# Kernel tuning notes

Measured on AMD Instinct MI355X. Metric: run time of the kernel, lower is better.

## Reference

```python
import jax, jax.numpy as jnp
import numpy as np

T, B, IN = 512, 256, 64
INNER = 20


def _lin_params(key, fan_in, fan_out):
    k1, k2 = jax.random.split(key)
    bound = 1.0 / np.sqrt(fan_in)
    w = jax.random.uniform(k1, (fan_out, fan_in), jnp.float32, -bound, bound)
    b = jax.random.uniform(k2, (fan_out,), jnp.float32, -bound, bound)
    return w, b


def _rnn_params(key, in_sz, hid):
    k1, k2, k3, k4 = jax.random.split(key, 4)
    bound = 1.0 / np.sqrt(hid)
    wih = jax.random.uniform(k1, (hid, in_sz), jnp.float32, -bound, bound)
    whh = jax.random.uniform(k2, (hid, hid), jnp.float32, -bound, bound)
    bih = jax.random.uniform(k3, (hid,), jnp.float32, -bound, bound)
    bhh = jax.random.uniform(k4, (hid,), jnp.float32, -bound, bound)
    return wih, whh, bih, bhh


def setup_inputs() -> dict:
    key = jax.random.key(0)
    ks = jax.random.split(key, 9)
    x = jax.random.normal(ks[0], (T, B, IN), jnp.float32)
    e_w1, e_b1 = _lin_params(ks[1], IN, 128)
    e_w2, e_b2 = _lin_params(ks[2], 128, 64)
    e_w3, e_b3 = _lin_params(ks[3], 64, 32)
    r1_wih, r1_whh, r1_bih, r1_bhh = _rnn_params(ks[4], 32, INNER)
    r2_wih, r2_whh, r2_bih, r2_bhh = _rnn_params(ks[5], INNER, 32)
    d_w1, d_b1 = _lin_params(ks[6], 32, 64)
    d_w2, d_b2 = _lin_params(ks[7], 64, 128)
    d_w3, d_b3 = _lin_params(ks[8], 128, IN)
    return dict(x=x,
                e_w1=e_w1, e_b1=e_b1, e_w2=e_w2, e_b2=e_b2, e_w3=e_w3, e_b3=e_b3,
                r1_wih=r1_wih, r1_whh=r1_whh, r1_bih=r1_bih, r1_bhh=r1_bhh,
                r2_wih=r2_wih, r2_whh=r2_whh, r2_bih=r2_bih, r2_bhh=r2_bhh,
                d_w1=d_w1, d_b1=d_b1, d_w2=d_w2, d_b2=d_b2, d_w3=d_w3, d_b3=d_b3)


def _rnn(x, wih, whh, bih, bhh):
    # x: (T, B, F); vanilla tanh RNN, h0 = 0. Returns all hidden states (T, B, H).
    # Precompute input projection for all timesteps in one GEMM.
    xp = jnp.einsum('tbf,hf->tbh', x, wih) + bih + bhh
    h0 = jnp.zeros((x.shape[1], whh.shape[0]), x.dtype)

    def step(h, xt):
        h = jnp.tanh(xt + h @ whh.T)
        return h, h

    _, out = jax.lax.scan(step, h0, xp)
    return out


def reference(x,
              e_w1, e_b1, e_w2, e_b2, e_w3, e_b3,
              r1_wih, r1_whh, r1_bih, r1_bhh,
              r2_wih, r2_whh, r2_bih, r2_bhh,
              d_w1, d_b1, d_w2, d_b2, d_w3, d_b3):
    relu = jax.nn.relu
    # encoder MLP
    h = relu(x @ e_w1.T + e_b1)
    h = relu(h @ e_w2.T + e_b2)
    h = relu(h @ e_w3.T + e_b3)
    # encoder RNN -> code (T, B, INNER)
    code = _rnn(h, r1_wih, r1_whh, r1_bih, r1_bhh)
    # decoder RNN then ReLU
    d = relu(_rnn(code, r2_wih, r2_whh, r2_bih, r2_bhh))
    d = relu(d @ d_w1.T + d_b1)
    d = relu(d @ d_w2.T + d_b2)
    return d @ d_w3.T + d_b3
```

## Files before the change

### kernel.cpp

```cpp
#include <hip/hip_runtime.h>

typedef _Float16 half8 __attribute__((ext_vector_type(8)));
typedef _Float16 half2_t __attribute__((ext_vector_type(2)));
typedef float f32x4 __attribute__((ext_vector_type(4)));

#define MFMA16(a, b, c) __builtin_amdgcn_mfma_f32_16x16x32_f16((a), (b), (c), 0, 0, 0)

__device__ __forceinline__ float exp2_fast(float x) {
#if __has_builtin(__builtin_amdgcn_exp2f)
    return __builtin_amdgcn_exp2f(x);
#else
    return exp2f(x);
#endif
}

__device__ __forceinline__ float tanh_fast(float x) {
    x = fminf(x, 22.f);
    float e = exp2_fast(2.885390082f * x);
    return (e - 1.f) * __builtin_amdgcn_rcpf(e + 1.f);
}

__device__ __forceinline__ float dot2f(unsigned a, unsigned b, float c) {
#if __has_builtin(__builtin_amdgcn_fdot2)
    return __builtin_amdgcn_fdot2(__builtin_bit_cast(half2_t, a),
                                  __builtin_bit_cast(half2_t, b), c, false);
#else
    float d;
    asm("v_dot2_f32_f16 %0, %1, %2, %3" : "=v"(d) : "v"(a), "v"(b), "v"(c));
    return d;
#endif
}


__global__ __launch_bounds__(256) void prep_kernel(
    const float* __restrict__ e_w1, const float* __restrict__ e_w3,
    const float* __restrict__ r1_wih, const float* __restrict__ e_w2,
    const float* __restrict__ d_w1, const float* __restrict__ d_w2,
    const float* __restrict__ d_w3,
    const float* __restrict__ r1_whh, const float* __restrict__ r2_wih,
    const float* __restrict__ r2_whh,
    const float* __restrict__ r2_bih, const float* __restrict__ r2_bhh,
    _Float16* __restrict__ enc_img, _Float16* __restrict__ w2img,
    _Float16* __restrict__ dec_img, _Float16* __restrict__ dw3img,
    unsigned* __restrict__ rnn_img)
{
    int i = blockIdx.x * 256 + threadIdx.x;
    if (i < 8192) {
        int r = i >> 6, c = i & 63;
        enc_img[r * 72 + c] = (_Float16)e_w1[i];
    } else if (i < 10240) {
        int j = i - 8192; int r = j >> 6, c = j & 63;
        enc_img[9216 + r * 72 + c] = (_Float16)e_w3[j];
    } else if (i < 10880) {
        int j = i - 10240; int r = j >> 5, c = j & 31;
        enc_img[11520 + r * 40 + c] = (_Float16)r1_wih[j];
    } else if (i < 19072) {
        int j = i - 10880;
        w2img[j] = (_Float16)e_w2[j];
    } else if (i < 21120) {
        int j = i - 19072; int r = j >> 5, c = j & 31;
        dec_img[r * 40 + c] = (_Float16)d_w1[j];
    } else if (i < 29312) {
        int j = i - 21120; int r = j >> 6, c = j & 63;
        dec_img[2560 + r * 72 + c] = (_Float16)d_w2[j];
    } else if (i < 37504) {
        int j = i - 29312;
        dw3img[j] = (_Float16)d_w3[j];
    } else if (i < 39552) {
        int j = i - 37504;
        int row = j >> 5, c = j & 31;
        unsigned val = 0;
        if (c == 26) {
            float b = (row < 32) ? (r2_bih[row] + r2_bhh[row]) : 0.f;
            val = __builtin_bit_cast(unsigned, b);
        } else {
            float v0 = 0.f, v1 = 0.f;
            if (row < 32) {
                if (c < 10)      { v0 = r2_wih[row * 20 + 2*c]; v1 = r2_wih[row * 20 + 2*c + 1]; }
                else if (c < 26) { int k = c - 10;
                                   v0 = r2_whh[row * 32 + 2*k]; v1 = r2_whh[row * 32 + 2*k + 1]; }
            } else if (row < 52) {
                int uu = row - 32;
                if (c < 10)      { v0 = r1_whh[uu * 20 + 2*c]; v1 = r1_whh[uu * 20 + 2*c + 1]; }
            }
            unsigned lo = (unsigned)__builtin_bit_cast(unsigned short, (_Float16)v0);
            unsigned hi = (unsigned)__builtin_bit_cast(unsigned short, (_Float16)v1);
            val = lo | (hi << 16);
        }
        rnn_img[j] = val;
    }
}

__global__ __launch_bounds__(256) void enc_kernel(
    const float* __restrict__ x,
    const float* __restrict__ eb1, const float* __restrict__ eb2,
    const float* __restrict__ eb3,
    const float* __restrict__ r1bih, const float* __restrict__ r1bhh,
    const _Float16* __restrict__ enc_img, const _Float16* __restrict__ w2img,
    float* __restrict__ xp1)
{
    extern __shared__ char smem[];
    _Float16* Wl    = (_Float16*)smem;
    _Float16* a2buf = (_Float16*)(smem + 25600);
    _Float16* a1buf = (_Float16*)(smem + 34816);
    _Float16* a3buf = (_Float16*)(smem + 52224);

    const int tid = threadIdx.x;
    {
        const uint4* src = (const uint4*)enc_img;
        uint4* dst = (uint4*)smem;
        #pragma unroll
        for (int i = 0; i < 7; ++i) {
            int idx = i * 256 + tid;
            if (idx < 1600) dst[idx] = src[idx];
        }
    }
    __syncthreads();

    const int lane = tid & 63;
    const int wv   = tid >> 6;
    const int l15  = lane & 15;
    const int kg   = lane >> 4;
    const int rowA  = blockIdx.x * 64 + wv * 16 + l15;
    const int rowDl = wv * 16 + kg * 4;
    const int rowDg = blockIdx.x * 64 + rowDl;

    half8 a0, a1f;
    {
        const float* xr = x + (size_t)rowA * 64 + kg * 8;
        f32x4 p0 = *(const f32x4*)(xr);
        f32x4 p1 = *(const f32x4*)(xr + 4);
        f32x4 p2 = *(const f32x4*)(xr + 32);
        f32x4 p3 = *(const f32x4*)(xr + 36);
        #pragma unroll
        for (int j = 0; j < 4; ++j) {
            a0[j]    = (_Float16)p0[j];
            a0[j+4]  = (_Float16)p1[j];
            a1f[j]   = (_Float16)p2[j];
            a1f[j+4] = (_Float16)p3[j];
        }
    }
    f32x4 acc1[8] = {};
    #pragma unroll
    for (int ct = 0; ct < 8; ++ct) {
        const _Float16* wp = Wl + (ct * 16 + l15) * 72 + kg * 8;
        half8 b0 = *(const half8*)(wp);
        half8 b1 = *(const half8*)(wp + 32);
        acc1[ct] = MFMA16(a0, b0, acc1[ct]);
        acc1[ct] = MFMA16(a1f, b1, acc1[ct]);
    }
    #pragma unroll
    for (int ct = 0; ct < 8; ++ct) {
        int col = ct * 16 + l15;
        float b = eb1[col];
        #pragma unroll
        for (int r = 0; r < 4; ++r) {
            float v = fmaxf(acc1[ct][r] + b, 0.f);
            a1buf[(rowDl + r) * 136 + col] = (_Float16)v;
        }
    }
    __syncthreads();

    half8 af[4];
    #pragma unroll
    for (int kt = 0; kt < 4; ++kt)
        af[kt] = *(const half8*)(a1buf + (wv * 16 + l15) * 136 + kt * 32 + kg * 8);
    f32x4 acc2[4] = {};
    #pragma unroll
    for (int ct = 0; ct < 4; ++ct) {
        const _Float16* wp = w2img + (ct * 16 + l15) * 128 + kg * 8;
        #pragma unroll
        for (int kt = 0; kt < 4; ++kt) {
            half8 b = *(const half8*)(wp + kt * 32);
            acc2[ct] = MFMA16(af[kt], b, acc2[ct]);
        }
    }
    #pragma unroll
    for (int ct = 0; ct < 4; ++ct) {
        int col = ct * 16 + l15;
        float b = eb2[col];
        #pragma unroll
        for (int r = 0; r < 4; ++r) {
            float v = fmaxf(acc2[ct][r] + b, 0.f);
            a2buf[(rowDl + r) * 72 + col] = (_Float16)v;
        }
    }
    __syncthreads();

    half8 c0 = *(const half8*)(a2buf + (wv * 16 + l15) * 72 + kg * 8);
    half8 c1 = *(const half8*)(a2buf + (wv * 16 + l15) * 72 + 32 + kg * 8);
    f32x4 acc3[2] = {};
    #pragma unroll
    for (int ct = 0; ct < 2; ++ct) {
        const _Float16* wp = Wl + 9216 + (ct * 16 + l15) * 72 + kg * 8;
        half8 b0 = *(const half8*)(wp);
        half8 b1 = *(const half8*)(wp + 32);
        acc3[ct] = MFMA16(c0, b0, acc3[ct]);
        acc3[ct] = MFMA16(c1, b1, acc3[ct]);
    }
    #pragma unroll
    for (int ct = 0; ct < 2; ++ct) {
        int col = ct * 16 + l15;
        float b = eb3[col];
        #pragma unroll
        for (int r = 0; r < 4; ++r) {
            float v = fmaxf(acc3[ct][r] + b, 0.f);
            a3buf[(rowDl + r) * 40 + col] = (_Float16)v;
        }
    }
    __syncthreads();

    half8 d0 = *(const half8*)(a3buf + (wv * 16 + l15) * 40 + kg * 8);
    f32x4 acc4[2] = {};
    #pragma unroll
    for (int ct = 0; ct < 2; ++ct) {
        const _Float16* wp = Wl + 11520 + (ct * 16 + l15) * 40 + kg * 8;
        half8 b0 = *(const half8*)(wp);
        acc4[ct] = MFMA16(d0, b0, acc4[ct]);
    }
    #pragma unroll
    for (int ct = 0; ct < 2; ++ct) {
        int col = ct * 16 + l15;
        if (col < 20) {
            float bs = r1bih[col] + r1bhh[col];
            #pragma unroll
            for (int r = 0; r < 4; ++r)
                xp1[(size_t)(rowDg + r) * 20 + col] = acc4[ct][r] + bs;
        }
    }
}

__global__ __launch_bounds__(64) void rnn_kernel(
    const float* __restrict__ xp1,
    const unsigned* __restrict__ rnn_img,
    _Float16* __restrict__ dbuf)
{
    const int lane  = threadIdx.x & 63;
    const int batch = blockIdx.x;

    unsigned w[26];
    float base_b;
    {
        const unsigned* wr = rnn_img + lane * 32;
        #pragma unroll
        for (int i = 0; i < 6; ++i) {
            uint4 q = *(const uint4*)(wr + i * 4);
            w[i*4+0] = q.x; w[i*4+1] = q.y; w[i*4+2] = q.z; w[i*4+3] = q.w;
        }
        uint4 q = *(const uint4*)(wr + 24);
        w[24] = q.x; w[25] = q.y;
        base_b = __builtin_bit_cast(float, q.z);
    }

    const bool isB = lane < 32;
    int ua = lane - 32;
    if (ua < 0 || ua > 19) ua = 0;
    const float* xcol = xp1 + (size_t)batch * 20 + ua;

    const size_t DUMP_ELEMS = 4198400;
    _Float16* dst = isB ? (dbuf + (size_t)batch * 32 + lane)
                        : (dbuf + DUMP_ELEMS + (size_t)batch * 64 + lane);
    const size_t dstride = isB ? 8192 : 0;

    const unsigned sel = (lane & 1) ? 0x01000504u : 0x05040100u;
    unsigned hs[26];

    {
        float x0 = xcol[0];
        float h0 = isB ? 0.f : tanh_fast(x0);
        _Float16 h16 = (_Float16)h0;
        unsigned own  = (unsigned)__builtin_bit_cast(unsigned short, h16);
        unsigned dppv = (unsigned)__builtin_amdgcn_update_dpp(0, (int)own, 0xB1, 0xF, 0xF, false);
        unsigned pk   = __builtin_amdgcn_perm(dppv, own, sel);
        #pragma unroll
        for (int i = 0; i < 10; ++i) hs[i]    = (unsigned)__builtin_amdgcn_readlane((int)pk, 32 + 2*i);
        #pragma unroll
        for (int i = 0; i < 16; ++i) hs[10+i] = (unsigned)__builtin_amdgcn_readlane((int)pk, 2*i);
    }

    float xr[8];
    #pragma unroll
    for (int j = 0; j < 8; ++j)
        xr[j] = xcol[(size_t)(1 + j) * 5120];

    #pragma unroll 1
    for (int t0 = 0; t0 < 512; t0 += 8) {
        #pragma unroll
        for (int j = 0; j < 8; ++j) {
            const int t = t0 + j;
            float a0 = isB ? base_b : xr[j];
            float a1 = 0.f, a2 = 0.f, a3 = 0.f, a4 = 0.f, a5 = 0.f, a6 = 0.f, a7 = 0.f;
            a0 = dot2f(w[0],  hs[0],  a0);
            a1 = dot2f(w[1],  hs[1],  a1);
            a2 = dot2f(w[2],  hs[2],  a2);
            a3 = dot2f(w[3],  hs[3],  a3);
            a4 = dot2f(w[4],  hs[4],  a4);
            a5 = dot2f(w[5],  hs[5],  a5);
            a6 = dot2f(w[6],  hs[6],  a6);
            a7 = dot2f(w[7],  hs[7],  a7);
            a0 = dot2f(w[8],  hs[8],  a0);
            a1 = dot2f(w[9],  hs[9],  a1);
            a2 = dot2f(w[10], hs[10], a2);
            a3 = dot2f(w[11], hs[11], a3);
            a4 = dot2f(w[12], hs[12], a4);
            a5 = dot2f(w[13], hs[13], a5);
            a6 = dot2f(w[14], hs[14], a6);
            a7 = dot2f(w[15], hs[15], a7);
            a0 = dot2f(w[16], hs[16], a0);
            a1 = dot2f(w[17], hs[17], a1);
            a2 = dot2f(w[18], hs[18], a2);
            a3 = dot2f(w[19], hs[19], a3);
            a4 = dot2f(w[20], hs[20], a4);
            a5 = dot2f(w[21], hs[21], a5);
            a6 = dot2f(w[22], hs[22], a6);
            a7 = dot2f(w[23], hs[23], a7);
            a0 = dot2f(w[24], hs[24], a0);
            a1 = dot2f(w[25], hs[25], a1);
            float r = ((a0 + a1) + (a2 + a3)) + ((a4 + a5) + (a6 + a7));
            float h = tanh_fast(r);
            _Float16 h16 = (_Float16)h;

            _Float16 z = (_Float16)0.f;
            *dst = (h16 > z) ? h16 : z;
            dst += dstride;

            unsigned own  = (unsigned)__builtin_bit_cast(unsigned short, h16);
            unsigned dppv = (unsigned)__builtin_amdgcn_update_dpp(0, (int)own, 0xB1, 0xF, 0xF, false);
            unsigned pk   = __builtin_amdgcn_perm(dppv, own, sel);
            #pragma unroll
            for (int i = 0; i < 10; ++i) hs[i]    = (unsigned)__builtin_amdgcn_readlane((int)pk, 32 + 2*i);
            #pragma unroll
            for (int i = 0; i < 16; ++i) hs[10+i] = (unsigned)__builtin_amdgcn_readlane((int)pk, 2*i);

            xr[j] = xcol[(size_t)(t + 9) * 5120];
        }
    }
}

__global__ __launch_bounds__(256) void dec_kernel(
    const _Float16* __restrict__ dbuf,
    const float* __restrict__ db1, const float* __restrict__ db2,
    const float* __restrict__ db3,
    const _Float16* __restrict__ dec_img, const _Float16* __restrict__ dw3img,
    float* __restrict__ out)
{
    extern __shared__ char smem[];
    _Float16* Wl    = (_Float16*)smem;
    _Float16* a1buf = (_Float16*)(smem + 23552);
    _Float16* a2buf = (_Float16*)(smem + 32768);

    const int tid = threadIdx.x;
    {
        const uint4* src = (const uint4*)dec_img;
        uint4* dst = (uint4*)smem;
        #pragma unroll
        for (int i = 0; i < 6; ++i) {
            int idx = i * 256 + tid;
            if (idx < 1472) dst[idx] = src[idx];
        }
    }
    __syncthreads();

    const int lane = tid & 63;
    const int wv   = tid >> 6;
    const int l15  = lane & 15;
    const int kg   = lane >> 4;
    const int rowA  = blockIdx.x * 64 + wv * 16 + l15;
    const int rowDl = wv * 16 + kg * 4;
    const int rowDg = blockIdx.x * 64 + rowDl;

    half8 a0 = *(const half8*)(dbuf + (size_t)rowA * 32 + kg * 8);
    f32x4 acc1[4] = {};
    #pragma unroll
    for (int ct = 0; ct < 4; ++ct) {
        half8 b = *(const half8*)(Wl + (ct * 16 + l15) * 40 + kg * 8);
        acc1[ct] = MFMA16(a0, b, acc1[ct]);
    }
    #pragma unroll
    for (int ct = 0; ct < 4; ++ct) {
        int col = ct * 16 + l15;
        float b = db1[col];
        #pragma unroll
        for (int r = 0; r < 4; ++r) {
            float v = fmaxf(acc1[ct][r] + b, 0.f);
            a1buf[(rowDl + r) * 72 + col] = (_Float16)v;
        }
    }
    __syncthreads();

    half8 af0 = *(const half8*)(a1buf + (wv * 16 + l15) * 72 + kg * 8);
    half8 af1 = *(const half8*)(a1buf + (wv * 16 + l15) * 72 + 32 + kg * 8);
    f32x4 acc2[8] = {};
    #pragma unroll
    for (int ct = 0; ct < 8; ++ct) {
        const _Float16* wp = Wl + 2560 + (ct * 16 + l15) * 72 + kg * 8;
        half8 b0 = *(const half8*)(wp);
        half8 b1 = *(const half8*)(wp + 32);
        acc2[ct] = MFMA16(af0, b0, acc2[ct]);
        acc2[ct] = MFMA16(af1, b1, acc2[ct]);
    }
    #pragma unroll
    for (int ct = 0; ct < 8; ++ct) {
        int col = ct * 16 + l15;
        float b = db2[col];
        #pragma unroll
        for (int r = 0; r < 4; ++r) {
            float v = fmaxf(acc2[ct][r] + b, 0.f);
            a2buf[(rowDl + r) * 136 + col] = (_Float16)v;
        }
    }
    __syncthreads();

    half8 cf[4];
    #pragma unroll
    for (int kt = 0; kt < 4; ++kt)
        cf[kt] = *(const half8*)(a2buf + (wv * 16 + l15) * 136 + kt * 32 + kg * 8);
    f32x4 acc3[4] = {};
    #pragma unroll
    for (int ct = 0; ct < 4; ++ct) {
        const _Float16* wp = dw3img + (ct * 16 + l15) * 128 + kg * 8;
        #pragma unroll
        for (int kt = 0; kt < 4; ++kt) {
            half8 b = *(const half8*)(wp + kt * 32);
            acc3[ct] = MFMA16(cf[kt], b, acc3[ct]);
        }
    }
    #pragma unroll
    for (int ct = 0; ct < 4; ++ct) {
        int col = ct * 16 + l15;
        float b = db3[col];
        #pragma unroll
        for (int r = 0; r < 4; ++r)
            out[(size_t)(rowDg + r) * 64 + col] = acc3[ct][r] + b;
    }
}

extern "C" void kernel_launch(void* const* d_in, const int* in_sizes, int n_in,
                              void* d_out, int out_size, void* d_ws, size_t ws_size,
                              hipStream_t stream) {
    const float* x      = (const float*)d_in[0];
    const float* e_w1   = (const float*)d_in[1];
    const float* e_b1   = (const float*)d_in[2];
    const float* e_w2   = (const float*)d_in[3];
    const float* e_b2   = (const float*)d_in[4];
    const float* e_w3   = (const float*)d_in[5];
    const float* e_b3   = (const float*)d_in[6];
    const float* r1_wih = (const float*)d_in[7];
    const float* r1_whh = (const float*)d_in[8];
    const float* r1_bih = (const float*)d_in[9];
    const float* r1_bhh = (const float*)d_in[10];
    const float* r2_wih = (const float*)d_in[11];
    const float* r2_whh = (const float*)d_in[12];
    const float* r2_bih = (const float*)d_in[13];
    const float* r2_bhh = (const float*)d_in[14];
    const float* d_w1   = (const float*)d_in[15];
    const float* d_b1   = (const float*)d_in[16];
    const float* d_w2   = (const float*)d_in[17];
    const float* d_b2   = (const float*)d_in[18];
    const float* d_w3   = (const float*)d_in[19];
    const float* d_b3   = (const float*)d_in[20];

    char* ws = (char*)d_ws;
    _Float16* enc_img = (_Float16*)(ws + 0);
    _Float16* w2img   = (_Float16*)(ws + 25600);
    _Float16* dec_img = (_Float16*)(ws + 41984);
    _Float16* dw3img  = (_Float16*)(ws + 65536);
    float*    xp1     = (float*)(ws + 81920);
    _Float16* dbuf    = (_Float16*)(ws + 10567680);
    unsigned* rnn_img = (unsigned*)(ws + 18956288);

    prep_kernel<<<155, 256, 0, stream>>>(e_w1, e_w3, r1_wih, e_w2, d_w1, d_w2, d_w3,
                                         r1_whh, r2_wih, r2_whh, r2_bih, r2_bhh,
                                         enc_img, w2img, dec_img, dw3img, rnn_img);
    enc_kernel<<<2048, 256, 57344, stream>>>(x, e_b1, e_b2, e_b3, r1_bih, r1_bhh,
                                             enc_img, w2img, xp1);
    rnn_kernel<<<256, 64, 0, stream>>>(xp1, rnn_img, dbuf);
    dec_kernel<<<2048, 256, 50176, stream>>>(dbuf, d_b1, d_b2, d_b3, dec_img, dw3img,
                                             (float*)d_out);
}
```

Measured before the change: 157.1 us.

## Interleave two batch chains per wave in RNN kernel and broadcast hidden state via LDS

The recurrent kernel now processes two independent batch elements per 64-lane wave, which halves the grid to 128 blocks and interleaves two dependency chains to hide latency. The hidden-state broadcast changes from DPP plus 26 readlanes to LDS writes followed by vector LDS reads. The accumulation tree is reduced from eight partial sums to four. Risks: with a single wave, LDS write-then-read ordering relies on in-order wave execution and has no barrier; halving the block count leaves more CUs idle, and LDS latency sits on the serial critical path.

```diff
diff --git a/kernel.cpp b/kernel.cpp
--- a/kernel.cpp
+++ b/kernel.cpp
@@ -3,6 +3,8 @@
 typedef _Float16 half8 __attribute__((ext_vector_type(8)));
 typedef _Float16 half2_t __attribute__((ext_vector_type(2)));
 typedef float f32x4 __attribute__((ext_vector_type(4)));
+typedef unsigned u32x4 __attribute__((ext_vector_type(4)));
+typedef unsigned u32x2 __attribute__((ext_vector_type(2)));
 
 #define MFMA16(a, b, c) __builtin_amdgcn_mfma_f32_16x16x32_f16((a), (b), (c), 0, 0, 0)
 
@@ -29,6 +31,29 @@
     asm("v_dot2_f32_f16 %0, %1, %2, %3" : "=v"(d) : "v"(a), "v"(b), "v"(c));
     return d;
 #endif
+}
+
+__device__ __forceinline__ float cell(const unsigned* w,
+                                      u32x4 h0, u32x4 h1, u32x4 h2,
+                                      u32x4 h3, u32x4 h4, u32x4 h5, u32x2 h6,
+                                      float init)
+{
+    float a0 = dot2f(w[0], h0[0], init);
+    float a1 = dot2f(w[1], h0[1], 0.f);
+    float a2 = dot2f(w[2], h0[2], 0.f);
+    float a3 = dot2f(w[3], h0[3], 0.f);
+    a0 = dot2f(w[4],  h1[0], a0); a1 = dot2f(w[5],  h1[1], a1);
+    a2 = dot2f(w[6],  h1[2], a2); a3 = dot2f(w[7],  h1[3], a3);
+    a0 = dot2f(w[8],  h2[0], a0); a1 = dot2f(w[9],  h2[1], a1);
+    a2 = dot2f(w[10], h2[2], a2); a3 = dot2f(w[11], h2[3], a3);
+    a0 = dot2f(w[12], h3[0], a0); a1 = dot2f(w[13], h3[1], a1);
+    a2 = dot2f(w[14], h3[2], a2); a3 = dot2f(w[15], h3[3], a3);
+    a0 = dot2f(w[16], h4[0], a0); a1 = dot2f(w[17], h4[1], a1);
+    a2 = dot2f(w[18], h4[2], a2); a3 = dot2f(w[19], h4[3], a3);
+    a0 = dot2f(w[20], h5[0], a0); a1 = dot2f(w[21], h5[1], a1);
+    a2 = dot2f(w[22], h5[2], a2); a3 = dot2f(w[23], h5[3], a3);
+    a0 = dot2f(w[24], h6[0], a0); a1 = dot2f(w[25], h6[1], a1);
+    return (a0 + a1) + (a2 + a3);
 }
 
 
@@ -235,8 +260,11 @@
     const unsigned* __restrict__ rnn_img,
     _Float16* __restrict__ dbuf)
 {
-    const int lane  = threadIdx.x & 63;
-    const int batch = blockIdx.x;
+    __shared__ _Float16 hbuf[256];
+
+    const int lane = threadIdx.x & 63;
+    const int bA = blockIdx.x * 2;
+    const int bB = bA + 1;
 
     unsigned w[26];
     float base_b;
@@ -255,84 +283,70 @@
     const bool isB = lane < 32;
     int ua = lane - 32;
     if (ua < 0 || ua > 19) ua = 0;
-    const float* xcol = xp1 + (size_t)batch * 20 + ua;
+    const float* xcolA = xp1 + (size_t)bA * 20 + ua;
+    const float* xcolB = xp1 + (size_t)bB * 20 + ua;
+
+    const bool valid = lane < 52;
+    const int hidx = isB ? (20 + lane) : (lane - 32);
+    const int wrA = valid ? hidx : 192;
+    const int wrB = valid ? (64 + hidx) : 193;
 
     const size_t DUMP_ELEMS = 4198400;
-    _Float16* dst = isB ? (dbuf + (size_t)batch * 32 + lane)
-                        : (dbuf + DUMP_ELEMS + (size_t)batch * 64 + lane);
+    _Float16* dstA = isB ? (dbuf + (size_t)bA * 32 + lane)
+                         : (dbuf + DUMP_ELEMS + (size_t)bA * 64 + lane);
+    _Float16* dstB = isB ? (dbuf + (size_t)bB * 32 + lane)
+                         : (dbuf + DUMP_ELEMS + (size_t)bB * 64 + lane);
     const size_t dstride = isB ? 8192 : 0;
 
-    const unsigned sel = (lane & 1) ? 0x01000504u : 0x05040100u;
-    unsigned hs[26];
-
     {
-        float x0 = xcol[0];
-        float h0 = isB ? 0.f : tanh_fast(x0);
-        _Float16 h16 = (_Float16)h0;
-        unsigned own  = (unsigned)__builtin_bit_cast(unsigned short, h16);
-        unsigned dppv = (unsigned)__builtin_amdgcn_update_dpp(0, (int)own, 0xB1, 0xF, 0xF, false);
-        unsigned pk   = __builtin_amdgcn_perm(dppv, own, sel);
-        #pragma unroll
-        for (int i = 0; i < 10; ++i) hs[i]    = (unsigned)__builtin_amdgcn_readlane((int)pk, 32 + 2*i);
-        #pragma unroll
-        for (int i = 0; i < 16; ++i) hs[10+i] = (unsigned)__builtin_amdgcn_readlane((int)pk, 2*i);
-    }
-
-    float xr[8];
-    #pragma unroll
-    for (int j = 0; j < 8; ++j)
-        xr[j] = xcol[(size_t)(1 + j) * 5120];
+        float h0a = isB ? 0.f : tanh_fast(xcolA[0]);
+        float h0b = isB ? 0.f : tanh_fast(xcolB[0]);
+        hbuf[wrA] = (_Float16)h0a;
+        hbuf[wrB] = (_Float16)h0b;
+    }
+
+    const u32x4* hpA = (const u32x4*)&hbuf[0];
+    const u32x4* hpB = (const u32x4*)&hbuf[64];
+    u32x4 hA0 = hpA[0], hA1 = hpA[1], hA2 = hpA[2], hA3 = hpA[3], hA4 = hpA[4], hA5 = hpA[5];
+    u32x2 hA6 = *(const u32x2*)&hbuf[48];
+    u32x4 hB0 = hpB[0], hB1 = hpB[1], hB2 = hpB[2], hB3 = hpB[3], hB4 = hpB[4], hB5 = hpB[5];
+    u32x2 hB6 = *(const u32x2*)&hbuf[64 + 48];
+
+    float xrA[8], xrB[8];
+    #pragma unroll
+    for (int j = 0; j < 8; ++j) {
+        xrA[j] = xcolA[(size_t)(1 + j) * 5120];
+        xrB[j] = xcolB[(size_t)(1 + j) * 5120];
+    }
 
     #pragma unroll 1
     for (int t0 = 0; t0 < 512; t0 += 8) {
         #pragma unroll
         for (int j = 0; j < 8; ++j) {
             const int t = t0 + j;
-            float a0 = isB ? base_b : xr[j];
-            float a1 = 0.f, a2 = 0.f, a3 = 0.f, a4 = 0.f, a5 = 0.f, a6 = 0.f, a7 = 0.f;
-            a0 = dot2f(w[0],  hs[0],  a0);
-            a1 = dot2f(w[1],  hs[1],  a1);
-            a2 = dot2f(w[2],  hs[2],  a2);
-            a3 = dot2f(w[3],  hs[3],  a3);
-            a4 = dot2f(w[4],  hs[4],  a4);
-            a5 = dot2f(w[5],  hs[5],  a5);
-            a6 = dot2f(w[6],  hs[6],  a6);
-            a7 = dot2f(w[7],  hs[7],  a7);
-            a0 = dot2f(w[8],  hs[8],  a0);
-            a1 = dot2f(w[9],  hs[9],  a1);
-            a2 = dot2f(w[10], hs[10], a2);
-            a3 = dot2f(w[11], hs[11], a3);
-            a4 = dot2f(w[12], hs[12], a4);
-            a5 = dot2f(w[13], hs[13], a5);
-            a6 = dot2f(w[14], hs[14], a6);
-            a7 = dot2f(w[15], hs[15], a7);
-            a0 = dot2f(w[16], hs[16], a0);
-            a1 = dot2f(w[17], hs[17], a1);
-            a2 = dot2f(w[18], hs[18], a2);
-            a3 = dot2f(w[19], hs[19], a3);
-            a4 = dot2f(w[20], hs[20], a4);
-            a5 = dot2f(w[21], hs[21], a5);
-            a6 = dot2f(w[22], hs[22], a6);
-            a7 = dot2f(w[23], hs[23], a7);
-            a0 = dot2f(w[24], hs[24], a0);
-            a1 = dot2f(w[25], hs[25], a1);
-            float r = ((a0 + a1) + (a2 + a3)) + ((a4 + a5) + (a6 + a7));
-            float h = tanh_fast(r);
-            _Float16 h16 = (_Float16)h;
+            float initA = isB ? base_b : xrA[j];
+            float initB = isB ? base_b : xrB[j];
+            float rA = cell(w, hA0, hA1, hA2, hA3, hA4, hA5, hA6, initA);
+            float rB = cell(w, hB0, hB1, hB2, hB3, hB4, hB5, hB6, initB);
+            float hA = tanh_fast(rA);
+            float hB = tanh_fast(rB);
+            _Float16 hA16 = (_Float16)hA;
+            _Float16 hB16 = (_Float16)hB;
 
             _Float16 z = (_Float16)0.f;
-            *dst = (h16 > z) ? h16 : z;
-            dst += dstride;
-
-            unsigned own  = (unsigned)__builtin_bit_cast(unsigned short, h16);
-            unsigned dppv = (unsigned)__builtin_amdgcn_update_dpp(0, (int)own, 0xB1, 0xF, 0xF, false);
-            unsigned pk   = __builtin_amdgcn_perm(dppv, own, sel);
-            #pragma unroll
-            for (int i = 0; i < 10; ++i) hs[i]    = (unsigned)__builtin_amdgcn_readlane((int)pk, 32 + 2*i);
-            #pragma unroll
-            for (int i = 0; i < 16; ++i) hs[10+i] = (unsigned)__builtin_amdgcn_readlane((int)pk, 2*i);
-
-            xr[j] = xcol[(size_t)(t + 9) * 5120];
+            *dstA = (hA16 > z) ? hA16 : z;  dstA += dstride;
+            *dstB = (hB16 > z) ? hB16 : z;  dstB += dstride;
+
+            hbuf[wrA] = hA16;
+            hbuf[wrB] = hB16;
+
+            hA0 = hpA[0]; hA1 = hpA[1]; hA2 = hpA[2]; hA3 = hpA[3]; hA4 = hpA[4]; hA5 = hpA[5];
+            hA6 = *(const u32x2*)&hbuf[48];
+            hB0 = hpB[0]; hB1 = hpB[1]; hB2 = hpB[2]; hB3 = hpB[3]; hB4 = hpB[4]; hB5 = hpB[5];
+            hB6 = *(const u32x2*)&hbuf[64 + 48];
+
+            xrA[j] = xcolA[(size_t)(t + 9) * 5120];
+            xrB[j] = xcolB[(size_t)(t + 9) * 5120];
         }
     }
 }
@@ -474,7 +488,7 @@
                                          enc_img, w2img, dec_img, dw3img, rnn_img);
     enc_kernel<<<2048, 256, 57344, stream>>>(x, e_b1, e_b2, e_b3, r1_bih, r1_bhh,
                                              enc_img, w2img, xp1);
-    rnn_kernel<<<256, 64, 0, stream>>>(xp1, rnn_img, dbuf);
+    rnn_kernel<<<128, 64, 0, stream>>>(xp1, rnn_img, dbuf);
     dec_kernel<<<2048, 256, 50176, stream>>>(dbuf, d_b1, d_b2, d_b3, dec_img, dw3img,
                                              (float*)d_out);
 }
```

Measured after the change: 240.0 us. 52.8% more time.
